# Performance work log

Hardware: AMD Instinct MI355X
Metric: run time of the kernel (lower is better)

## Reference

```python
import jax, jax.numpy as jnp
import numpy as np

INPUT_SIZE = 1024
HIDDEN_SIZE = 1024
BATCH = 2048
EPS = 1e-5


def setup_inputs() -> dict:
    key = jax.random.key(0)
    ks = jax.random.split(key, 7)
    H = HIDDEN_SIZE
    # torch Linear default init: U(-1/sqrt(fan_in), 1/sqrt(fan_in))
    bi = 1.0 / np.sqrt(INPUT_SIZE)
    bh = 1.0 / np.sqrt(H)
    W_ih = jax.random.uniform(ks[0], (4 * H, INPUT_SIZE), jnp.float32, -bi, bi)
    W_hh = jax.random.uniform(ks[1], (4 * H, H), jnp.float32, -bh, bh)
    # biases filled to 0, forget slice [H:2H] to forget_bias=0 -> all zeros
    b_ih = jnp.zeros((4 * H,), jnp.float32)
    b_hh = jnp.zeros((4 * H,), jnp.float32)
    ln_w = jnp.ones((H,), jnp.float32)
    ln_b = jnp.zeros((H,), jnp.float32)
    x = jax.random.normal(ks[2], (BATCH, INPUT_SIZE), jnp.float32)
    h = jax.random.normal(ks[3], (BATCH, H), jnp.float32)
    c = jax.random.normal(ks[4], (BATCH, H), jnp.float32)
    return {"x": x, "h": h, "c": c, "W_ih": W_ih, "b_ih": b_ih,
            "W_hh": W_hh, "b_hh": b_hh, "ln_w": ln_w, "ln_b": ln_b}


def reference(x, h, c, W_ih, b_ih, W_hh, b_hh, ln_w, ln_b):
    H = HIDDEN_SIZE
    # dual linear: [B, 4H]
    preact = x @ W_ih.T + b_ih + h @ W_hh.T + b_hh
    gates = jax.nn.sigmoid(preact[:, :3 * H])
    g_t = jnp.tanh(preact[:, 3 * H:])
    i_t = gates[:, :H]
    f_t = gates[:, H:2 * H]
    o_t = gates[:, 2 * H:3 * H]
    c_t = c * f_t + i_t * g_t
    # LayerNorm over last dim
    mu = jnp.mean(c_t, axis=-1, keepdims=True)
    var = jnp.mean(jnp.square(c_t - mu), axis=-1, keepdims=True)
    c_t = (c_t - mu) / jnp.sqrt(var + EPS) * ln_w + ln_b
    h_t = o_t * jnp.tanh(c_t)
    return (h_t, c_t)
```

## Files before the change

### kernel.cpp

```cpp
#include <hip/hip_runtime.h>
#include <hip/hip_fp16.h>
#include <stdint.h>

#define H 1024
#define BATCH 2048
#define KDIM 2048
#define NDIM 4096
#define EPS 1e-5f

#define BM 128
#define BN 128
#define BK 256

typedef __attribute__((ext_vector_type(4))) int i32x4;

__device__ __forceinline__ float fast_sig(float x) {
  x = fminf(30.f, fmaxf(-30.f, x));
  float e = __expf(x);
  return e / (e + 1.f);
}

__device__ __forceinline__ float fast_tanh(float x) {
  x = fminf(15.f, fmaxf(-15.f, x));
  float e = __expf(2.f * x);
  return (e - 1.f) / (e + 1.f);
}

__global__ __launch_bounds__(256) void quant_kernel(
    const float* __restrict__ x, const float* __restrict__ h,
    const float* __restrict__ Wih, const float* __restrict__ Whh,
    char* __restrict__ Ai8, char* __restrict__ Bi8,
    float* __restrict__ sA, float* __restrict__ sB) {
  const int r = blockIdx.x;
  const int t = threadIdx.x;
  const float* s0;
  const float* s1;
  char* dst;
  float* sOut;
  if (r < BATCH) {
    s0 = x + (size_t)r * H;
    s1 = h + (size_t)r * H;
    dst = Ai8 + (size_t)r * KDIM;
    sOut = sA + r;
  } else {
    const int rb = r - BATCH;
    s0 = Wih + (size_t)rb * H;
    s1 = Whh + (size_t)rb * H;
    dst = Bi8 + (size_t)rb * KDIM;
    sOut = sB + rb;
  }
  const float* src = (t < 128) ? (s0 + t * 8) : (s1 + (t - 128) * 8);
  float4 v0 = *(const float4*)src;
  float4 v1 = *(const float4*)(src + 4);
  float vv[8] = {v0.x, v0.y, v0.z, v0.w, v1.x, v1.y, v1.z, v1.w};

  float m = 0.f;
#pragma unroll
  for (int i = 0; i < 8; ++i) m = fmaxf(m, fabsf(vv[i]));
#pragma unroll
  for (int off = 32; off > 0; off >>= 1) m = fmaxf(m, __shfl_xor(m, off));
  __shared__ float red[4];
  if ((t & 63) == 0) red[t >> 6] = m;
  __syncthreads();
  m = fmaxf(fmaxf(red[0], red[1]), fmaxf(red[2], red[3]));
  m = fmaxf(m, 1e-20f);
  if (t == 0) *sOut = m * (1.0f / 127.0f);
  const float inv = 127.0f / m;

  char out[8];
#pragma unroll
  for (int i = 0; i < 8; ++i) {
    int qi = (int)rintf(vv[i] * inv);
    qi = max(-127, min(127, qi));
    out[i] = (char)qi;
  }
  *(int2*)(dst + t * 8) = *(const int2*)out;
}

__device__ __forceinline__ void load_lds16(const void* g, void* l) {
  __builtin_amdgcn_global_load_lds(
      (const __attribute__((address_space(1))) void*)g,
      (__attribute__((address_space(3))) void*)l, 16, 0, 0);
}

__global__ __launch_bounds__(256, 2) void gemm_kernel(
    const char* __restrict__ A8,
    const char* __restrict__ B8,
    const float* __restrict__ sA, const float* __restrict__ sB,
    __half* __restrict__ P) {
  __shared__ char sAt[BM * BK];
  __shared__ char sBt[BN * BK];

  const int tid = threadIdx.x;
  const int wave = tid >> 6;
  const int lane = tid & 63;
  const int m0 = blockIdx.y * BM;
  const int n0 = blockIdx.x * BN;
  const int wr = (wave >> 1) * 64;
  const int wc = (wave & 1) * 64;

  const int frow = lane & 15;
  const int klane = lane >> 4;
  const int rxor = (frow & 7);

  i32x4 acc[4][4] = {};

  const int NT = KDIM / BK;

  for (int t = 0; t < NT; ++t) {
    const int k0 = t * BK;
#pragma unroll
    for (int p = 0; p < 8; ++p) {
      const int rg = wave * 32 + p * 4;
      const int srcoff = (((lane & 15) ^ ((4 * (p & 1)) + (lane >> 4))) << 4);
      load_lds16(A8 + (size_t)(m0 + rg + (lane >> 4)) * KDIM + k0 + srcoff,
                 sAt + rg * BK);
      load_lds16(B8 + (size_t)(n0 + rg + (lane >> 4)) * KDIM + k0 + srcoff,
                 sBt + rg * BK);
    }
    asm volatile("s_waitcnt vmcnt(0)" ::: "memory");
    __syncthreads();

#pragma unroll
    for (int ks = 0; ks < 4; ++ks) {
      const int coff = (((ks * 4 + klane) ^ rxor) << 4);
      i32x4 a[4], b[4];
#pragma unroll
      for (int i = 0; i < 4; ++i) {
        a[i] = *(const i32x4*)(sAt + (wr + i * 16 + frow) * BK + coff);
        b[i] = *(const i32x4*)(sBt + (wc + i * 16 + frow) * BK + coff);
      }
      __builtin_amdgcn_s_setprio(1);
#pragma unroll
      for (int i = 0; i < 4; ++i)
#pragma unroll
        for (int j = 0; j < 4; ++j)
          acc[i][j] =
              __builtin_amdgcn_mfma_i32_16x16x64_i8(a[i], b[j], acc[i][j], 0, 0, 0);
      __builtin_amdgcn_s_setprio(0);
    }

    __syncthreads();
  }

  const int crow = (lane >> 4) << 2;
  const int ccol = lane & 15;
  float scA[4][4], scB[4];
#pragma unroll
  for (int j = 0; j < 4; ++j) scB[j] = sB[n0 + wc + j * 16 + ccol];
#pragma unroll
  for (int i = 0; i < 4; ++i)
#pragma unroll
    for (int r = 0; r < 4; ++r) scA[i][r] = sA[m0 + wr + i * 16 + crow + r];

#pragma unroll
  for (int i = 0; i < 4; ++i)
#pragma unroll
    for (int j = 0; j < 4; ++j) {
      __half* cp = P + (size_t)(m0 + wr + i * 16 + crow) * NDIM + (n0 + wc + j * 16 + ccol);
#pragma unroll
      for (int r = 0; r < 4; ++r)
        cp[(size_t)r * NDIM] = __float2half((float)acc[i][j][r] * scA[i][r] * scB[j]);
    }
}

__global__ __launch_bounds__(256) void epilogue_kernel(
    const __half* __restrict__ P, const float* __restrict__ c_in,
    const float* __restrict__ b_ih, const float* __restrict__ b_hh,
    const float* __restrict__ ln_w, const float* __restrict__ ln_b,
    float* __restrict__ h_out, float* __restrict__ c_out) {
  const int m = blockIdx.x;
  const int t = threadIdx.x;
  const int j = t << 2;
  const __half* r0 = P + (size_t)m * NDIM;

  float pre[4][4];
#pragma unroll
  for (int g = 0; g < 4; ++g) {
    ushort4 u0 = *(const ushort4*)(r0 + g * H + j);
    float4 bi = *(const float4*)(b_ih + g * H + j);
    float4 bh = *(const float4*)(b_hh + g * H + j);
    pre[g][0] = __half2float(*(__half*)&u0.x) + bi.x + bh.x;
    pre[g][1] = __half2float(*(__half*)&u0.y) + bi.y + bh.y;
    pre[g][2] = __half2float(*(__half*)&u0.z) + bi.z + bh.z;
    pre[g][3] = __half2float(*(__half*)&u0.w) + bi.w + bh.w;
  }
  float4 ci = *(const float4*)(c_in + (size_t)m * H + j);

  float cr[4], vo[4];
  float s = 0.f, q = 0.f;
#pragma unroll
  for (int r = 0; r < 4; ++r) {
    float iv = fast_sig(pre[0][r]);
    float fv = fast_sig(pre[1][r]);
    float ov = fast_sig(pre[2][r]);
    float gv = fast_tanh(pre[3][r]);
    float cv = ((const float*)&ci)[r] * fv + iv * gv;
    cr[r] = cv;
    vo[r] = ov;
    s += cv;
    q += cv * cv;
  }

#pragma unroll
  for (int off = 32; off > 0; off >>= 1) {
    s += __shfl_xor(s, off);
    q += __shfl_xor(q, off);
  }
  __shared__ float red[8];
  const int wv = t >> 6, ln = t & 63;
  if (ln == 0) {
    red[wv] = s;
    red[wv + 4] = q;
  }
  __syncthreads();
  s = red[0] + red[1] + red[2] + red[3];
  q = red[4] + red[5] + red[6] + red[7];
  const float mu = s * (1.f / H);
  const float var = q * (1.f / H) - mu * mu;
  const float rstd = rsqrtf(var + EPS);

  float4 lw = *(const float4*)(ln_w + j);
  float4 lb = *(const float4*)(ln_b + j);
  float4 hov, cov;
#pragma unroll
  for (int r = 0; r < 4; ++r) {
    float cn = (cr[r] - mu) * rstd * ((const float*)&lw)[r] + ((const float*)&lb)[r];
    ((float*)&cov)[r] = cn;
    ((float*)&hov)[r] = vo[r] * fast_tanh(cn);
  }
  *(float4*)(h_out + (size_t)m * H + j) = hov;
  *(float4*)(c_out + (size_t)m * H + j) = cov;
}

extern "C" void kernel_launch(void* const* d_in, const int* in_sizes, int n_in,
                              void* d_out, int out_size, void* d_ws, size_t ws_size,
                              hipStream_t stream) {
  const float* x = (const float*)d_in[0];
  const float* h = (const float*)d_in[1];
  const float* c = (const float*)d_in[2];
  const float* Wih = (const float*)d_in[3];
  const float* b_ih = (const float*)d_in[4];
  const float* Whh = (const float*)d_in[5];
  const float* b_hh = (const float*)d_in[6];
  const float* ln_w = (const float*)d_in[7];
  const float* ln_b = (const float*)d_in[8];

  char* Ai8 = (char*)d_ws;
  char* Bi8 = (char*)d_ws + (4u << 20);
  float* sA = (float*)((char*)d_ws + (12u << 20));
  float* sB = (float*)((char*)d_ws + (12u << 20) + 32768);
  __half* P = (__half*)((char*)d_ws + (16u << 20));

  float* h_out = (float*)d_out;
  float* c_out = (float*)d_out + (size_t)BATCH * H;

  quant_kernel<<<BATCH + NDIM, 256, 0, stream>>>(x, h, Wih, Whh, Ai8, Bi8, sA, sB);
  dim3 g(NDIM / BN, BATCH / BM);
  gemm_kernel<<<g, 256, 0, stream>>>(Ai8, Bi8, sA, sB, P);
  epilogue_kernel<<<BATCH, 256, 0, stream>>>(P, c, b_ih, b_hh, ln_w, ln_b, h_out, c_out);
}
```

Measured before the change: 47.73 us.

## Interleave gate rows in weights and fuse gate activations into GEMM epilogue

The quantization kernel now writes weight rows in gate-interleaved order (hidden*4+gate) and precomputes the combined bias. Because of that ordering, each GEMM tile holds all four gates for 32 hidden units. The GEMM therefore stages its float results in LDS, applies sigmoid/tanh and the cell update itself, and writes only half-precision cell and output-gate values. This replaces the full 4H half-precision preactivation round trip with two H-wide half arrays, which removes most epilogue memory traffic. The cost is a larger LDS footprint (about 65KB) that may lower GEMM occupancy, plus an extra syncthreads and an LDS epilogue.

```diff
diff --git a/kernel.cpp b/kernel.cpp
--- a/kernel.cpp
+++ b/kernel.cpp
@@ -29,14 +29,17 @@
 __global__ __launch_bounds__(256) void quant_kernel(
     const float* __restrict__ x, const float* __restrict__ h,
     const float* __restrict__ Wih, const float* __restrict__ Whh,
+    const float* __restrict__ b_ih, const float* __restrict__ b_hh,
     char* __restrict__ Ai8, char* __restrict__ Bi8,
-    float* __restrict__ sA, float* __restrict__ sB) {
+    float* __restrict__ sA, float* __restrict__ sB, float* __restrict__ bsum) {
   const int r = blockIdx.x;
   const int t = threadIdx.x;
   const float* s0;
   const float* s1;
   char* dst;
   float* sOut;
+  float bs = 0.f;
+  float* bOut = nullptr;
   if (r < BATCH) {
     s0 = x + (size_t)r * H;
     s1 = h + (size_t)r * H;
@@ -44,10 +47,15 @@
     sOut = sA + r;
   } else {
     const int rb = r - BATCH;
+    const int g = rb >> 10;
+    const int hh = rb & 1023;
+    const int rr = hh * 4 + g;
     s0 = Wih + (size_t)rb * H;
     s1 = Whh + (size_t)rb * H;
-    dst = Bi8 + (size_t)rb * KDIM;
-    sOut = sB + rb;
+    dst = Bi8 + (size_t)rr * KDIM;
+    sOut = sB + rr;
+    bs = b_ih[rb] + b_hh[rb];
+    bOut = bsum + rr;
   }
   const float* src = (t < 128) ? (s0 + t * 8) : (s1 + (t - 128) * 8);
   float4 v0 = *(const float4*)src;
@@ -64,7 +72,10 @@
   __syncthreads();
   m = fmaxf(fmaxf(red[0], red[1]), fmaxf(red[2], red[3]));
   m = fmaxf(m, 1e-20f);
-  if (t == 0) *sOut = m * (1.0f / 127.0f);
+  if (t == 0) {
+    *sOut = m * (1.0f / 127.0f);
+    if (bOut) *bOut = bs;
+  }
   const float inv = 127.0f / m;
 
   char out[8];
@@ -87,9 +98,12 @@
     const char* __restrict__ A8,
     const char* __restrict__ B8,
     const float* __restrict__ sA, const float* __restrict__ sB,
-    __half* __restrict__ P) {
-  __shared__ char sAt[BM * BK];
-  __shared__ char sBt[BN * BK];
+    const float* __restrict__ bsum, const float* __restrict__ c_in,
+    __half* __restrict__ cvg, __half* __restrict__ ovg) {
+  __shared__ __align__(16) char smem[66560];
+  char* sAt = smem;
+  char* sBt = smem + 32768;
+  float* pf = (float*)smem;
 
   const int tid = threadIdx.x;
   const int wave = tid >> 6;
@@ -145,63 +159,68 @@
 
   const int crow = (lane >> 4) << 2;
   const int ccol = lane & 15;
-  float scA[4][4], scB[4];
-#pragma unroll
-  for (int j = 0; j < 4; ++j) scB[j] = sB[n0 + wc + j * 16 + ccol];
+  float scA_[4][4], scB_[4], bs_[4];
+#pragma unroll
+  for (int j = 0; j < 4; ++j) {
+    scB_[j] = sB[n0 + wc + j * 16 + ccol];
+    bs_[j] = bsum[n0 + wc + j * 16 + ccol];
+  }
 #pragma unroll
   for (int i = 0; i < 4; ++i)
 #pragma unroll
-    for (int r = 0; r < 4; ++r) scA[i][r] = sA[m0 + wr + i * 16 + crow + r];
+    for (int r = 0; r < 4; ++r) scA_[i][r] = sA[m0 + wr + i * 16 + crow + r];
 
 #pragma unroll
   for (int i = 0; i < 4; ++i)
 #pragma unroll
     for (int j = 0; j < 4; ++j) {
-      __half* cp = P + (size_t)(m0 + wr + i * 16 + crow) * NDIM + (n0 + wc + j * 16 + ccol);
+      const int col = wc + j * 16 + ccol;
 #pragma unroll
       for (int r = 0; r < 4; ++r)
-        cp[(size_t)r * NDIM] = __float2half((float)acc[i][j][r] * scA[i][r] * scB[j]);
+        pf[(wr + i * 16 + crow + r) * 130 + col] =
+            (float)acc[i][j][r] * scA_[i][r] * scB_[j] + bs_[j];
     }
-}
-
-__global__ __launch_bounds__(256) void epilogue_kernel(
-    const __half* __restrict__ P, const float* __restrict__ c_in,
-    const float* __restrict__ b_ih, const float* __restrict__ b_hh,
+  __syncthreads();
+
+  const int mrow = tid >> 1;
+  const int hq = tid & 1;
+  const size_t orow = (size_t)(m0 + mrow) * H + blockIdx.x * 32;
+  const float* prow = pf + mrow * 130;
+#pragma unroll
+  for (int k = 0; k < 16; ++k) {
+    const int hl = hq * 16 + ((k + mrow) & 15);
+    float4 g4 = *(const float4*)(prow + hl * 4);
+    float cin = c_in[orow + hl];
+    float iv = fast_sig(g4.x);
+    float fv = fast_sig(g4.y);
+    float ov = fast_sig(g4.z);
+    float gv = fast_tanh(g4.w);
+    float cv = cin * fv + iv * gv;
+    cvg[orow + hl] = __float2half(cv);
+    ovg[orow + hl] = __float2half(ov);
+  }
+}
+
+__global__ __launch_bounds__(256) void ln_kernel(
+    const __half* __restrict__ cvg, const __half* __restrict__ ovg,
     const float* __restrict__ ln_w, const float* __restrict__ ln_b,
     float* __restrict__ h_out, float* __restrict__ c_out) {
   const int m = blockIdx.x;
   const int t = threadIdx.x;
   const int j = t << 2;
-  const __half* r0 = P + (size_t)m * NDIM;
-
-  float pre[4][4];
-#pragma unroll
-  for (int g = 0; g < 4; ++g) {
-    ushort4 u0 = *(const ushort4*)(r0 + g * H + j);
-    float4 bi = *(const float4*)(b_ih + g * H + j);
-    float4 bh = *(const float4*)(b_hh + g * H + j);
-    pre[g][0] = __half2float(*(__half*)&u0.x) + bi.x + bh.x;
-    pre[g][1] = __half2float(*(__half*)&u0.y) + bi.y + bh.y;
-    pre[g][2] = __half2float(*(__half*)&u0.z) + bi.z + bh.z;
-    pre[g][3] = __half2float(*(__half*)&u0.w) + bi.w + bh.w;
-  }
-  float4 ci = *(const float4*)(c_in + (size_t)m * H + j);
-
-  float cr[4], vo[4];
+  ushort4 uc = *(const ushort4*)(cvg + (size_t)m * H + j);
+  ushort4 uo = *(const ushort4*)(ovg + (size_t)m * H + j);
+  float cv[4] = {__half2float(*(__half*)&uc.x), __half2float(*(__half*)&uc.y),
+                 __half2float(*(__half*)&uc.z), __half2float(*(__half*)&uc.w)};
+  float ov[4] = {__half2float(*(__half*)&uo.x), __half2float(*(__half*)&uo.y),
+                 __half2float(*(__half*)&uo.z), __half2float(*(__half*)&uo.w)};
+
   float s = 0.f, q = 0.f;
 #pragma unroll
   for (int r = 0; r < 4; ++r) {
-    float iv = fast_sig(pre[0][r]);
-    float fv = fast_sig(pre[1][r]);
-    float ov = fast_sig(pre[2][r]);
-    float gv = fast_tanh(pre[3][r]);
-    float cv = ((const float*)&ci)[r] * fv + iv * gv;
-    cr[r] = cv;
-    vo[r] = ov;
-    s += cv;
-    q += cv * cv;
-  }
-
+    s += cv[r];
+    q += cv[r] * cv[r];
+  }
 #pragma unroll
   for (int off = 32; off > 0; off >>= 1) {
     s += __shfl_xor(s, off);
@@ -225,9 +244,9 @@
   float4 hov, cov;
 #pragma unroll
   for (int r = 0; r < 4; ++r) {
-    float cn = (cr[r] - mu) * rstd * ((const float*)&lw)[r] + ((const float*)&lb)[r];
+    float cn = (cv[r] - mu) * rstd * ((const float*)&lw)[r] + ((const float*)&lb)[r];
     ((float*)&cov)[r] = cn;
-    ((float*)&hov)[r] = vo[r] * fast_tanh(cn);
+    ((float*)&hov)[r] = ov[r] * fast_tanh(cn);
   }
   *(float4*)(h_out + (size_t)m * H + j) = hov;
   *(float4*)(c_out + (size_t)m * H + j) = cov;
@@ -250,13 +269,16 @@
   char* Bi8 = (char*)d_ws + (4u << 20);
   float* sA = (float*)((char*)d_ws + (12u << 20));
   float* sB = (float*)((char*)d_ws + (12u << 20) + 32768);
-  __half* P = (__half*)((char*)d_ws + (16u << 20));
+  float* bsum = (float*)((char*)d_ws + (12u << 20) + 98304);
+  __half* cvg = (__half*)((char*)d_ws + (16u << 20));
+  __half* ovg = (__half*)((char*)d_ws + (20u << 20));
 
   float* h_out = (float*)d_out;
   float* c_out = (float*)d_out + (size_t)BATCH * H;
 
-  quant_kernel<<<BATCH + NDIM, 256, 0, stream>>>(x, h, Wih, Whh, Ai8, Bi8, sA, sB);
+  quant_kernel<<<BATCH + NDIM, 256, 0, stream>>>(x, h, Wih, Whh, b_ih, b_hh,
+                                                 Ai8, Bi8, sA, sB, bsum);
   dim3 g(NDIM / BN, BATCH / BM);
-  gemm_kernel<<<g, 256, 0, stream>>>(Ai8, Bi8, sA, sB, P);
-  epilogue_kernel<<<BATCH, 256, 0, stream>>>(P, c, b_ih, b_hh, ln_w, ln_b, h_out, c_out);
-}
+  gemm_kernel<<<g, 256, 0, stream>>>(Ai8, Bi8, sA, sB, bsum, c, cvg, ovg);
+  ln_kernel<<<BATCH, 256, 0, stream>>>(cvg, ovg, ln_w, ln_b, h_out, c_out);
+}
```

New measurement: 61.89 us. +29.7%, slower.
